# Kernel tuning notes

Measured on AMD Instinct MI355X. Metric: run time of the kernel, lower is better.

The kernel has to match this reference:

```python
import jax, jax.numpy as jnp
import numpy as np

OUT_SIZE = 14
CUTOFF = 0.2
VAR0 = 4            # var[0], mixin_factor = 0.0 -> current std = var[0]
BETA = 4.0
N_SQ = OUT_SIZE * OUT_SIZE
TAU = 0.5 / N_SQ
BATCH = 256
CHANNELS = 512


def _gkern_np(kernlen, std, vmin, vmax):
    n = np.arange(kernlen) - (kernlen - 1) / 2.0
    w = np.exp(-(n ** 2) / (2.0 * std * std))
    g = np.outer(w, w)
    return g * (vmax - vmin) + vmin


def _build_templates():
    n = OUT_SIZE
    base = _gkern_np(2 * n - 1, VAR0, -CUTOFF, 1.0)
    base = np.maximum(base, 0.0) * 2.0 - 1.0
    base = TAU * np.clip(BETA * base / n, -1.0, None)  # clamp(min=-1) only
    # unfold(0,n,1).unfold(1,n,1).reshape(-1,n,n) == sliding windows, row-major
    t = np.lib.stride_tricks.sliding_window_view(base, (n, n)).reshape(-1, n, n)
    t = np.flip(t, axis=0).copy()  # torch.flip(templates, dims=(0,))
    templates_f = jnp.asarray(t, jnp.float32)                    # (n^2, n, n)
    neg = -TAU * jnp.ones((1, n, n), jnp.float32)
    templates_b = jnp.concatenate([templates_f, neg], axis=0)    # (n^2+1, n, n)
    alpha = N_SQ / (1.0 + N_SQ)
    p_T = jnp.asarray(
        np.array([alpha / N_SQ] * N_SQ + [1.0 - alpha], np.float32))  # (n^2+1,)
    return templates_f, templates_b, p_T


def setup_inputs() -> dict:
    key = jax.random.key(0)
    templates_f, templates_b, p_T = _build_templates()
    x = jax.random.normal(key, (BATCH, CHANNELS, OUT_SIZE, OUT_SIZE), jnp.float32)
    return {"x": x, "templates_f": templates_f,
            "templates_b": templates_b, "p_T": p_T}


def reference(x, templates_f, templates_b, p_T):
    B, C, H, W = x.shape
    tau = 0.5 / (H * W)
    # max_pool2d with kernel == full spatial extent -> flat argmax per (b, c)
    idx = jnp.argmax(x.reshape(B, C, H * W), axis=-1)            # (B, C) int
    sel = templates_f[idx]                                       # (B, C, H, W)
    mask = sel / jnp.max(sel)                                    # global max
    mask = jax.nn.relu(mask - CUTOFF) / CUTOFF
    x_masked = x * mask
    # local loss (mutual-information style) on the masked activations
    tr_x_T = jnp.einsum('bcwh,twh->cbt', x_masked * tau, templates_b)  # (C,B,T)
    p_x_T = jax.nn.softmax(tr_x_T, axis=1)                       # softmax over b
    p_x = jnp.einsum('t,cbt->cb', p_T, p_x_T)                    # (C, B)
    log_ratio = jnp.log(p_x_T / p_x[:, :, None])                 # (C, B, T)
    p_x_T_log = jnp.einsum('cbt,cbt->ct', p_x_T, log_ratio)      # (C, T)
    loss = -jnp.einsum('t,ct->c', p_T, p_x_T_log)                # (C,)
    return x_masked, mask, loss
```

## Files before the change

kernel.cpp:

```cpp
#include <hip/hip_runtime.h>

#define BB 256
#define CCH 512
#define HW 196
#define TT 197
#define TROWS 208
#define NFRAG (13 * 7)
#define ASHORTS (NFRAG * 64 * 8)
#define RPW 32
#define F4PW (RPW * 49)

typedef __attribute__((ext_vector_type(8))) short bf16x8;
typedef __attribute__((ext_vector_type(4))) float f32x4;

__device__ __forceinline__ unsigned short f2bf(float f) {
    union { float f; unsigned u; } v; v.f = f;
    unsigned r = v.u + 0x7FFFu + ((v.u >> 16) & 1u);
    return (unsigned short)(r >> 16);
}

__global__ void prep(const float* __restrict__ tf, const float* __restrict__ tb,
                     float* __restrict__ wsf, unsigned short* __restrict__ tb_bf) {
    if (blockIdx.x < 182) {
        int i = blockIdx.x * 256 + threadIdx.x;
        int frag = i >> 9;
        int s    = i & 511;
        int mt = frag / 7, kt = frag % 7;
        int lane = s >> 3, j = s & 7;
        int r = mt * 16 + (lane & 15);
        int k = kt * 32 + (lane >> 4) * 8 + j;
        const float tau = 0.5f / 196.0f;
        float v = (r < TT && k < HW) ? tb[r * HW + k] * tau : 0.0f;
        tb_bf[i] = f2bf(v);
    } else {
        __shared__ float red[256];
        float m = -1e30f;
        for (int i = threadIdx.x; i < HW * HW; i += 256) m = fmaxf(m, tf[i]);
        red[threadIdx.x] = m;
        __syncthreads();
        for (int s = 128; s > 0; s >>= 1) {
            if (threadIdx.x < s) red[threadIdx.x] = fmaxf(red[threadIdx.x], red[threadIdx.x + s]);
            __syncthreads();
        }
        if (threadIdx.x == 0) wsf[0] = red[0];
    }
}

extern "C" __global__ __launch_bounds__(256, 4)
void k_stream3(const float* __restrict__ x, const float* __restrict__ tf,
               const float* __restrict__ wsf,
               float* __restrict__ xm_out, float* __restrict__ mask_out)
{
    __shared__ float xs[RPW * HW];
    __shared__ int   biL[RPW];

    const int tid = threadIdx.x;
    const float rg = 1.0f / wsf[0];
    const size_t base4 = (size_t)blockIdx.x * F4PW;
    const f32x4* x4 = (const f32x4*)x + base4;
    f32x4* xs4 = (f32x4*)xs;

    f32x4 u[7];
    #pragma unroll
    for (int k = 0; k < 6; ++k) u[k] = x4[tid + k * 256];
    if (tid < F4PW - 1536) u[6] = x4[tid + 1536];
    #pragma unroll
    for (int k = 0; k < 6; ++k) xs4[tid + k * 256] = u[k];
    if (tid < F4PW - 1536) xs4[tid + 1536] = u[6];
    __syncthreads();

    {
        const int row = tid >> 3;
        const int o   = tid & 7;
        float bv = -__builtin_inff(); int bi = 0;
        #pragma unroll
        for (int t = 0; t < 7; ++t) {
            const int j = o + 8 * t;
            if (j < 49) {
                f32x4 xv = xs4[row * 49 + j];
                const int k0 = j * 4;
                #pragma unroll
                for (int e = 0; e < 4; ++e) {
                    float v = xv[e];
                    if (v > bv) { bv = v; bi = k0 + e; }
                }
            }
        }
        #pragma unroll
        for (int m = 1; m <= 4; m <<= 1) {
            float ov = __shfl_xor(bv, m, 64);
            int   oi = __shfl_xor(bi, m, 64);
            if (ov > bv || (ov == bv && oi < bi)) { bv = ov; bi = oi; }
        }
        if (o == 0) biL[row] = bi;
    }
    __syncthreads();

    const f32x4* tf4 = (const f32x4*)tf;
    f32x4* xm4 = (f32x4*)xm_out + base4;
    f32x4* mk4 = (f32x4*)mask_out + base4;

    #pragma unroll
    for (int k = 0; k < 7; ++k) {
        const int idx = tid + k * 256;
        if (k < 6 || idx < F4PW) {
            const int rl = idx / 49;
            const int j  = idx - rl * 49;
            const int bi = biL[rl];
            f32x4 sel = tf4[bi * 49 + j];
            f32x4 xv  = u[k];
            f32x4 mk, xm;
            #pragma unroll
            for (int e = 0; e < 4; ++e) {
                float m = fmaxf(sel[e] * rg - 0.2f, 0.0f) * 5.0f;
                mk[e] = m;
                xm[e] = xv[e] * m;
            }
            xm4[idx] = xm;
            mk4[idx] = mk;
        }
    }
}

extern "C" __global__ __launch_bounds__(1024)
void k_gemm_loss(const float* __restrict__ xm, const float* __restrict__ pT,
                 const unsigned short* __restrict__ tb_bf,
                 float* __restrict__ loss_out)
{
    extern __shared__ char smem[];
    unsigned short* Alds = (unsigned short*)smem;
    float* s_part = (float*)(smem + ASHORTS * 2);
    float* rAs    = s_part + 16 * TROWS;
    float* pTs    = rAs + TROWS;
    float* red    = pTs + TROWS;

    const int c    = blockIdx.x;
    const int tid  = threadIdx.x;
    const int lane = tid & 63;
    const int w    = tid >> 6;
    const int l15  = lane & 15, lg = lane >> 4;

    {
        const f32x4* src = (const f32x4*)tb_bf;
        f32x4* dst = (f32x4*)Alds;
        #pragma unroll
        for (int it = 0; it < 6; ++it) {
            int idx = tid + it * 1024;
            if (idx < ASHORTS / 8) dst[idx] = src[idx];
        }
    }
    if (tid < TROWS) pTs[tid] = (tid < TT) ? pT[tid] : 0.0f;

    const int b = w * 16 + l15;
    const float* xrow = xm + ((size_t)b * CCH + c) * HW;

    bf16x8 fr[7];
    #pragma unroll
    for (int kt = 0; kt < 6; ++kt) {
        f32x4 u0 = *(const f32x4*)(xrow + kt * 32 + lg * 8);
        f32x4 u1 = *(const f32x4*)(xrow + kt * 32 + lg * 8 + 4);
        #pragma unroll
        for (int e = 0; e < 4; ++e) {
            fr[kt][e]     = (short)f2bf(u0[e]);
            fr[kt][e + 4] = (short)f2bf(u1[e]);
        }
    }
    fr[6] = (bf16x8){0, 0, 0, 0, 0, 0, 0, 0};
    if (lg == 0) {
        f32x4 u0 = *(const f32x4*)(xrow + 192);
        #pragma unroll
        for (int e = 0; e < 4; ++e) fr[6][e] = (short)f2bf(u0[e]);
    }

    __syncthreads();

    f32x4 acc[13];
    #pragma unroll
    for (int mt = 0; mt < 13; ++mt) acc[mt] = (f32x4){0.f, 0.f, 0.f, 0.f};

    const unsigned short* Abase = Alds + lane * 8;
    #pragma unroll
    for (int kt = 0; kt < 7; ++kt) {
        const bf16x8 bfrag = fr[kt];
        #pragma unroll
        for (int mt = 0; mt < 13; ++mt) {
            bf16x8 afrag = *(const bf16x8*)(Abase + (mt * 7 + kt) * 512);
            acc[mt] = __builtin_amdgcn_mfma_f32_16x16x32_bf16(afrag, bfrag, acc[mt], 0, 0, 0);
        }
    }

    float* sp = s_part + w * TROWS;
    #pragma unroll
    for (int mt = 0; mt < 13; ++mt) {
        #pragma unroll
        for (int e = 0; e < 4; ++e) acc[mt][e] = __expf(acc[mt][e]);
        f32x4 s = acc[mt];
        #pragma unroll
        for (int m = 1; m <= 8; m <<= 1) {
            #pragma unroll
            for (int e = 0; e < 4; ++e) s[e] += __shfl_xor(s[e], m, 64);
        }
        if (l15 == 0) *(f32x4*)(sp + mt * 16 + lg * 4) = s;
    }
    __syncthreads();
    if (tid < TROWS) {
        float s = 0.f;
        #pragma unroll
        for (int w2 = 0; w2 < 16; ++w2) s += s_part[w2 * TROWS + tid];
        rAs[tid] = 1.0f / s;
    }
    __syncthreads();

    float px = 0.f;
    #pragma unroll
    for (int mt = 0; mt < 13; ++mt) {
        const int t0 = mt * 16 + lg * 4;
        f32x4 ra = *(const f32x4*)(rAs + t0);
        f32x4 pt = *(const f32x4*)(pTs + t0);
        #pragma unroll
        for (int e = 0; e < 4; ++e) {
            float p = acc[mt][e] * ra[e];
            acc[mt][e] = p;
            px += pt[e] * p;
        }
    }
    px += __shfl_xor(px, 16, 64);
    px += __shfl_xor(px, 32, 64);
    const float rpx = 1.0f / px;

    float part = 0.f;
    #pragma unroll
    for (int mt = 0; mt < 13; ++mt) {
        const int t0 = mt * 16 + lg * 4;
        f32x4 pt = *(const f32x4*)(pTs + t0);
        #pragma unroll
        for (int e = 0; e < 4; ++e) {
            float p = acc[mt][e];
            part += pt[e] * p * __logf(p * rpx);
        }
    }
    #pragma unroll
    for (int off = 32; off >= 1; off >>= 1) part += __shfl_xor(part, off, 64);
    if (lane == 0) red[w] = part;
    __syncthreads();
    if (tid == 0) {
        float s = 0.f;
        #pragma unroll
        for (int w2 = 0; w2 < 16; ++w2) s += red[w2];
        loss_out[c] = -s;
    }
}

extern "C" void kernel_launch(void* const* d_in, const int* in_sizes, int n_in,
                              void* d_out, int out_size, void* d_ws, size_t ws_size,
                              hipStream_t stream) {
    const float* x  = (const float*)d_in[0];
    const float* tf = (const float*)d_in[1];
    const float* tb = (const float*)d_in[2];
    const float* pT = (const float*)d_in[3];

    const size_t NOUT = (size_t)BB * CCH * HW;
    float* xm_out = (float*)d_out;
    float* mk_out = xm_out + NOUT;
    float* ls_out = mk_out + NOUT;

    float* wsf = (float*)d_ws;
    unsigned short* tb_bf = (unsigned short*)((char*)d_ws + 64);

    prep<<<183, 256, 0, stream>>>(tf, tb, wsf, tb_bf);
    k_stream3<<<(BB * CCH) / RPW, 256, 0, stream>>>(x, tf, wsf, xm_out, mk_out);

    const size_t SMEM = (size_t)ASHORTS * 2 + 16 * TROWS * 4
                      + TROWS * 4 + TROWS * 4 + 16 * 4;
    (void)hipFuncSetAttribute((const void*)k_gemm_loss,
                              hipFuncAttributeMaxDynamicSharedMemorySize, (int)SMEM);
    k_gemm_loss<<<dim3(CCH), dim3(1024), SMEM, stream>>>(xm_out, pT, tb_bf, ls_out);
}
```

Measured before the change: 140.5 us.

## Stage template fragments through LDS in two halves to cut shared memory

Splits the bf16 template matrix into two halves (7 and 6 M-tiles) and loads them one after the other into a single smaller LDS buffer, running the MFMA loop on each half in turn. This roughly halves the GEMM kernel's LDS footprint so more workgroups might fit per CU. In exchange it adds two block-wide barriers and a second serialized global-to-LDS copy in the middle of the compute.

```diff
diff --git a/kernel.cpp b/kernel.cpp
--- a/kernel.cpp
+++ b/kernel.cpp
@@ -5,8 +5,10 @@
 #define HW 196
 #define TT 197
 #define TROWS 208
-#define NFRAG (13 * 7)
-#define ASHORTS (NFRAG * 64 * 8)
+#define H1FRAG (7 * 7)
+#define H2FRAG (6 * 7)
+#define H1SHORTS (H1FRAG * 512)
+#define H2SHORTS (H2FRAG * 512)
 #define RPW 32
 #define F4PW (RPW * 49)
 
@@ -129,7 +131,7 @@
 {
     extern __shared__ char smem[];
     unsigned short* Alds = (unsigned short*)smem;
-    float* s_part = (float*)(smem + ASHORTS * 2);
+    float* s_part = (float*)(smem + H1SHORTS * 2);
     float* rAs    = s_part + 16 * TROWS;
     float* pTs    = rAs + TROWS;
     float* red    = pTs + TROWS;
@@ -144,9 +146,9 @@
         const f32x4* src = (const f32x4*)tb_bf;
         f32x4* dst = (f32x4*)Alds;
         #pragma unroll
-        for (int it = 0; it < 6; ++it) {
+        for (int it = 0; it < 4; ++it) {
             int idx = tid + it * 1024;
-            if (idx < ASHORTS / 8) dst[idx] = src[idx];
+            if (idx < H1SHORTS / 8) dst[idx] = src[idx];
         }
     }
     if (tid < TROWS) pTs[tid] = (tid < TT) ? pT[tid] : 0.0f;
@@ -183,8 +185,31 @@
     for (int kt = 0; kt < 7; ++kt) {
         const bf16x8 bfrag = fr[kt];
         #pragma unroll
-        for (int mt = 0; mt < 13; ++mt) {
+        for (int mt = 0; mt < 7; ++mt) {
             bf16x8 afrag = *(const bf16x8*)(Abase + (mt * 7 + kt) * 512);
+            acc[mt] = __builtin_amdgcn_mfma_f32_16x16x32_bf16(afrag, bfrag, acc[mt], 0, 0, 0);
+        }
+    }
+
+    __syncthreads();
+
+    {
+        const f32x4* src = (const f32x4*)(tb_bf + H1SHORTS);
+        f32x4* dst = (f32x4*)Alds;
+        #pragma unroll
+        for (int it = 0; it < 3; ++it) {
+            int idx = tid + it * 1024;
+            if (idx < H2SHORTS / 8) dst[idx] = src[idx];
+        }
+    }
+    __syncthreads();
+
+    #pragma unroll
+    for (int kt = 0; kt < 7; ++kt) {
+        const bf16x8 bfrag = fr[kt];
+        #pragma unroll
+        for (int mt = 7; mt < 13; ++mt) {
+            bf16x8 afrag = *(const bf16x8*)(Abase + ((mt - 7) * 7 + kt) * 512);
             acc[mt] = __builtin_amdgcn_mfma_f32_16x16x32_bf16(afrag, bfrag, acc[mt], 0, 0, 0);
         }
     }
@@ -270,7 +295,8 @@
     prep<<<183, 256, 0, stream>>>(tf, tb, wsf, tb_bf);
     k_stream3<<<(BB * CCH) / RPW, 256, 0, stream>>>(x, tf, wsf, xm_out, mk_out);
 
-    const size_t SMEM = (size_t)ASHORTS * 2 + 16 * TROWS * 4
+    const size_t SMEM = (size_t)H1SHORTS * 2
+                      + 16 * TROWS * 4
                       + TROWS * 4 + TROWS * 4 + 16 * 4;
     (void)hipFuncSetAttribute((const void*)k_gemm_loss,
                               hipFuncAttributeMaxDynamicSharedMemorySize, (int)SMEM);
```

Result: no change. 140.4 us (-0.1%).
